# Kernel optimization log

Measured on AMD Instinct MI355X. Metric: run time of the kernel, lower is better.

The kernel has to match this reference:

```python
import jax, jax.numpy as jnp
import numpy as np

N, Z, H, W, R = 8192, 1024, 2048, 64, 8
SCALE = 1.0


def setup_inputs() -> dict:
    key = jax.random.key(0)
    ks = jax.random.split(key, 8)
    return {
        "z": jax.random.normal(ks[0], (N, Z), dtype=jnp.float32),
        "a_idx": jax.random.randint(ks[1], (N,), 0, W),
        "h_pre": jax.random.normal(ks[2], (N, H), dtype=jnp.float32),
        "out_pre": jax.random.normal(ks[3], (N, Z), dtype=jnp.float32),
        "a1": jax.random.normal(ks[4], (W, R, Z), dtype=jnp.float32) * 0.02,
        "b1": jax.random.normal(ks[5], (W, H, R), dtype=jnp.float32) * 0.02,
        "a2": jax.random.normal(ks[6], (W, R, H), dtype=jnp.float32) * 0.02,
        "b2": jax.random.normal(ks[7], (W, Z, R), dtype=jnp.float32) * 0.02,
    }


def reference(z, a_idx, h_pre, out_pre, a1, b1, a2, b2):
    # Gather per-token expert LoRA factors (faithful to torch indexing a1[a_idx])
    A1 = a1[a_idx]                                  # [N, R, Z]
    B1 = b1[a_idx]                                  # [N, H, R]
    t1 = jnp.einsum('nd,nrd->nr', z, A1)            # [N, R]
    d1 = jnp.einsum('nr,nhr->nh', t1, B1) * SCALE   # [N, H]
    h = jax.nn.silu(h_pre + d1)                     # [N, H]
    A2 = a2[a_idx]                                  # [N, R, H]
    B2 = b2[a_idx]                                  # [N, Z, R]
    t2 = jnp.einsum('nh,nrh->nr', h, A2)            # [N, R]
    d2 = jnp.einsum('nr,ndr->nd', t2, B2) * SCALE   # [N, Z]
    return out_pre + d2
```

## Files before the change

### kernel.cpp

```cpp
#include <hip/hip_runtime.h>
#include <stdint.h>


constexpr int Zd = 1024;
constexpr int Hd = 2048;
constexpr int Rr = 8;
constexpr int Wn = 64;
constexpr int TB = 16;
constexpr int TW = 2;
constexpr int NT = 512;
constexpr int HC = 256;
constexpr int NCHUNK = Hd / HC;
constexpr float kScale = 1.0f;


__global__ __launch_bounds__(1024) void bucket_kernel(
    const int* __restrict__ a_idx, int N, int* __restrict__ ws)
{
    __shared__ int hist[Wn];
    __shared__ int cursor[Wn];
    const int t = threadIdx.x;
    if (t < Wn) hist[t] = 0;
    __syncthreads();
    for (int i = t; i < N; i += 1024) atomicAdd(&hist[a_idx[i]], 1);
    __syncthreads();

    if (t < Wn) {
        const int c = hist[t];
        int scan = c;
#pragma unroll
        for (int off = 1; off < 64; off <<= 1) {
            const int v = __shfl_up(scan, off, 64);
            if (t >= off) scan += v;
        }
        const int base = scan - c;

        const int nb_e = (c + TB - 1) / TB;
        int bs = nb_e;
#pragma unroll
        for (int off = 1; off < 64; off <<= 1) {
            const int v = __shfl_up(bs, off, 64);
            if (t >= off) bs += v;
        }
        const int bstart = bs - nb_e;
        if (t == Wn - 1) ws[0] = bs;
        cursor[t] = base;

        int4* btab = (int4*)(ws + 16 + N);
        for (int s = 0, k = 0; s < c; s += TB, ++k)
            btab[bstart + k] = make_int4(t, base + s, min(TB, c - s), 0);
    }
    __syncthreads();
    int* order = ws + 16;
    for (int i = t; i < N; i += 1024) {
        const int pos = atomicAdd(&cursor[a_idx[i]], 1);
        order[pos] = i;
    }
}

__device__ __forceinline__ float wave_allreduce(float v) {
#pragma unroll
    for (int off = 1; off < 64; off <<= 1)
        v += __shfl_xor(v, off, 64);
    return v;
}

__device__ __forceinline__ float dot8(const float* t, float4 w0, float4 w1) {
    return fmaf(t[0], w0.x, fmaf(t[1], w0.y, fmaf(t[2], w0.z, fmaf(t[3], w0.w,
           fmaf(t[4], w1.x, fmaf(t[5], w1.y, fmaf(t[6], w1.z, t[7] * w1.w)))))));
}

__device__ __forceinline__ float silu(float x) {
    return x * __builtin_amdgcn_rcpf(1.f + __expf(-x));
}

__device__ __forceinline__ int swz(int o) {
    return o ^ (((o >> 7) & 7) << 4);
}

__device__ __forceinline__ void stage16(const void* g, void* l) {
    __builtin_amdgcn_global_load_lds(
        (const __attribute__((address_space(1))) uint32_t*)g,
        (__attribute__((address_space(3))) uint32_t*)l, 16, 0, 0);
}

#define WAITVM(N) asm volatile("s_waitcnt vmcnt(" #N ")" ::: "memory")
#define SYNC()    asm volatile("s_waitcnt lgkmcnt(0)\ns_barrier" ::: "memory")

__global__ __launch_bounds__(NT, 4) void lora_main(
    const float* __restrict__ z,
    const float* __restrict__ h_pre,
    const float* __restrict__ out_pre,
    const float* __restrict__ a1,
    const float* __restrict__ b1,
    const float* __restrict__ a2,
    const float* __restrict__ b2,
    float* __restrict__ out,
    const int* __restrict__ ws, int N)
{
    __shared__ float s_a1[Rr * Zd];
    __shared__ float s_b1[3][HC * Rr];
    __shared__ float s_a2[3][Rr * HC];

    const int cpx = gridDim.x >> 3;
    const int lb  = (blockIdx.x & 7) * cpx + (blockIdx.x >> 3);
    if (lb >= ws[0]) return;

    const int4 desc = ((const int4*)(ws + 16 + N))[lb];
    const int e = desc.x, start = desc.y, cnt = desc.z;
    const int* order = ws + 16;

    const int t    = threadIdx.x;
    const int wave = t >> 6;
    const int lane = t & 63;

    bool val[TW];
    int  tok[TW];
#pragma unroll
    for (int k = 0; k < TW; ++k) {
        const int idx = wave * TW + k;
        val[k] = (idx < cnt);
        tok[k] = order[start + (val[k] ? idx : 0)];
    }

    const char*  a1e = (const char*)(a1 + (size_t)e * (Rr * Zd));
    const char*  b1e = (const char*)(b1 + (size_t)e * (Hd * Rr));
    const float* a2e = a2 + (size_t)e * (Rr * Hd);
    const char*  b2e = (const char*)(b2 + (size_t)e * (Zd * Rr));

#pragma unroll
    for (int i = 0; i < 4; ++i) {
        const int o = (i * NT + t) * 16;
        stage16(a1e + o, (char*)s_a1 + (i * NT + wave * 64) * 16);
    }
#pragma unroll
    for (int c0 = 0; c0 < 2; ++c0) {
        const int o = t * 16;
        stage16(b1e + (size_t)(c0 * HC) * Rr * 4 + swz(o),
                (char*)s_b1[c0] + wave * 1024);
        stage16(a2e + wave * Hd + c0 * HC + lane * 4,
                (char*)s_a2[c0] + wave * 1024);
    }
    WAITVM(4);
    SYNC();

    float p[TW][Rr];
#pragma unroll
    for (int k = 0; k < TW; ++k)
#pragma unroll
        for (int r = 0; r < Rr; ++r) p[k][r] = 0.f;

#pragma unroll
    for (int i = 0; i < Zd / 4 / 64; ++i) {
        const int c = lane + i * 64;
        float4 zv[TW];
#pragma unroll
        for (int k = 0; k < TW; ++k)
            zv[k] = *(const float4*)(z + (size_t)tok[k] * Zd + 4 * c);
#pragma unroll
        for (int r = 0; r < Rr; ++r) {
            const float4 w = *(const float4*)(s_a1 + r * Zd + 4 * c);
#pragma unroll
            for (int k = 0; k < TW; ++k)
                p[k][r] = fmaf(zv[k].x, w.x, fmaf(zv[k].y, w.y,
                          fmaf(zv[k].z, w.z, fmaf(zv[k].w, w.w, p[k][r]))));
        }
    }
    float t1[TW][Rr];
#pragma unroll
    for (int k = 0; k < TW; ++k)
#pragma unroll
        for (int r = 0; r < Rr; ++r) t1[k][r] = wave_allreduce(p[k][r]);

    SYNC();

#pragma unroll
    for (int i = 0; i < 4; ++i) {
        const int o = (i * NT + t) * 16;
        stage16(b2e + swz(o), (char*)s_a1 + (i * NT + wave * 64) * 16);
    }

    float q[TW][Rr];
#pragma unroll
    for (int k = 0; k < TW; ++k)
#pragma unroll
        for (int r = 0; r < Rr; ++r) q[k][r] = 0.f;

#pragma unroll
    for (int kc = 0; kc < NCHUNK; ++kc) {
        if (kc < 2)      { WAITVM(6); }
        else if (kc < 7) { WAITVM(2); }
        else             { WAITVM(0); }
        SYNC();

        if (kc + 2 < NCHUNK) {
            const int nb = (kc + 2) % 3;
            const int hb = (kc + 2) * HC;
            const int o = t * 16;
            stage16(b1e + (size_t)hb * Rr * 4 + swz(o),
                    (char*)s_b1[nb] + wave * 1024);
            stage16(a2e + wave * Hd + hb + lane * 4,
                    (char*)s_a2[nb] + wave * 1024);
        }

        const int cur = kc % 3;
        const int cc = kc * 64 + lane;
        float4 hv[TW];
#pragma unroll
        for (int k = 0; k < TW; ++k)
            hv[k] = *(const float4*)(h_pre + (size_t)tok[k] * Hd + 4 * cc);

        float sv[TW][4];
#pragma unroll
        for (int j = 0; j < 4; ++j) {
            const int o0 = lane * 128 + j * 32;
            const float4 w0 = *(const float4*)((const char*)s_b1[cur] + swz(o0));
            const float4 w1 = *(const float4*)((const char*)s_b1[cur] + swz(o0 + 16));
#pragma unroll
            for (int k = 0; k < TW; ++k) {
                const float x = (&hv[k].x)[j] + dot8(t1[k], w0, w1) * kScale;
                sv[k][j] = silu(x);
            }
        }
#pragma unroll
        for (int r = 0; r < Rr; ++r) {
            const float4 aw = *(const float4*)(s_a2[cur] + r * HC + lane * 4);
#pragma unroll
            for (int k = 0; k < TW; ++k)
                q[k][r] = fmaf(sv[k][0], aw.x, fmaf(sv[k][1], aw.y,
                          fmaf(sv[k][2], aw.z, fmaf(sv[k][3], aw.w, q[k][r]))));
        }
    }

    float t2[TW][Rr];
#pragma unroll
    for (int k = 0; k < TW; ++k)
#pragma unroll
        for (int r = 0; r < Rr; ++r) t2[k][r] = wave_allreduce(q[k][r]) * kScale;

#pragma unroll
    for (int i = 0; i < Zd / 4 / 64; ++i) {
        const int c = lane + i * 64;
        float4 ov[TW];
#pragma unroll
        for (int k = 0; k < TW; ++k)
            ov[k] = *(const float4*)(out_pre + (size_t)tok[k] * Zd + 4 * c);
        float4 res[TW];
#pragma unroll
        for (int j = 0; j < 4; ++j) {
            const int o0 = c * 128 + j * 32;
            const float4 w0 = *(const float4*)((const char*)s_a1 + swz(o0));
            const float4 w1 = *(const float4*)((const char*)s_a1 + swz(o0 + 16));
#pragma unroll
            for (int k = 0; k < TW; ++k)
                (&res[k].x)[j] = (&ov[k].x)[j] + dot8(t2[k], w0, w1);
        }
#pragma unroll
        for (int k = 0; k < TW; ++k)
            if (val[k]) *(float4*)(out + (size_t)tok[k] * Zd + 4 * c) = res[k];
    }
}

extern "C" void kernel_launch(void* const* d_in, const int* in_sizes, int n_in,
                              void* d_out, int out_size, void* d_ws, size_t ws_size,
                              hipStream_t stream) {
    const float* z       = (const float*)d_in[0];
    const int*   a_idx   = (const int*)d_in[1];
    const float* h_pre   = (const float*)d_in[2];
    const float* out_pre = (const float*)d_in[3];
    const float* a1      = (const float*)d_in[4];
    const float* b1      = (const float*)d_in[5];
    const float* a2      = (const float*)d_in[6];
    const float* b2      = (const float*)d_in[7];
    float* out = (float*)d_out;

    const int N = in_sizes[1];

    bucket_kernel<<<1, 1024, 0, stream>>>(a_idx, N, (int*)d_ws);

    int nwg = N / TB + Wn;
    nwg = (nwg + 7) & ~7;
    lora_main<<<nwg, NT, 0, stream>>>(z, h_pre, out_pre, a1, b1, a2, b2, out,
                                      (const int*)d_ws, N);
}
```

Before: 57.83 us.

## Read A1/B2 directly from global, prefetch h_pre, vectorize bucket histogram

Removes the 32KB LDS staging of a1 and b2, so both are read straight from global/L2. This shrinks shared memory so more blocks fit per CU, and the occupancy hint rises from 4 to 6. h_pre rows are double-buffered one chunk ahead, and the vmcnt waits are retuned to match the new count of in-flight loads. The bucket kernel now reads a_idx as int4; the trade-off is redundant global reads of the weights by every wave and fewer registers per thread.

```diff
diff --git a/kernel.cpp b/kernel.cpp
--- a/kernel.cpp
+++ b/kernel.cpp
@@ -22,7 +22,12 @@
     const int t = threadIdx.x;
     if (t < Wn) hist[t] = 0;
     __syncthreads();
-    for (int i = t; i < N; i += 1024) atomicAdd(&hist[a_idx[i]], 1);
+    for (int i = t; i < N / 4; i += 1024) {
+        const int4 v = ((const int4*)a_idx)[i];
+        atomicAdd(&hist[v.x], 1); atomicAdd(&hist[v.y], 1);
+        atomicAdd(&hist[v.z], 1); atomicAdd(&hist[v.w], 1);
+    }
+    for (int i = (N & ~3) + t; i < N; i += 1024) atomicAdd(&hist[a_idx[i]], 1);
     __syncthreads();
 
     if (t < Wn) {
@@ -52,10 +57,15 @@
     }
     __syncthreads();
     int* order = ws + 16;
-    for (int i = t; i < N; i += 1024) {
-        const int pos = atomicAdd(&cursor[a_idx[i]], 1);
-        order[pos] = i;
-    }
+    for (int i = t; i < N / 4; i += 1024) {
+        const int4 v = ((const int4*)a_idx)[i];
+        order[atomicAdd(&cursor[v.x], 1)] = 4 * i + 0;
+        order[atomicAdd(&cursor[v.y], 1)] = 4 * i + 1;
+        order[atomicAdd(&cursor[v.z], 1)] = 4 * i + 2;
+        order[atomicAdd(&cursor[v.w], 1)] = 4 * i + 3;
+    }
+    for (int i = (N & ~3) + t; i < N; i += 1024)
+        order[atomicAdd(&cursor[a_idx[i]], 1)] = i;
 }
 
 __device__ __forceinline__ float wave_allreduce(float v) {
@@ -87,7 +97,7 @@
 #define WAITVM(N) asm volatile("s_waitcnt vmcnt(" #N ")" ::: "memory")
 #define SYNC()    asm volatile("s_waitcnt lgkmcnt(0)\ns_barrier" ::: "memory")
 
-__global__ __launch_bounds__(NT, 4) void lora_main(
+__global__ __launch_bounds__(NT, 6) void lora_main(
     const float* __restrict__ z,
     const float* __restrict__ h_pre,
     const float* __restrict__ out_pre,
@@ -98,7 +108,6 @@
     float* __restrict__ out,
     const int* __restrict__ ws, int N)
 {
-    __shared__ float s_a1[Rr * Zd];
     __shared__ float s_b1[3][HC * Rr];
     __shared__ float s_a2[3][Rr * HC];
 
@@ -123,16 +132,11 @@
         tok[k] = order[start + (val[k] ? idx : 0)];
     }
 
-    const char*  a1e = (const char*)(a1 + (size_t)e * (Rr * Zd));
-    const char*  b1e = (const char*)(b1 + (size_t)e * (Hd * Rr));
-    const float* a2e = a2 + (size_t)e * (Rr * Hd);
-    const char*  b2e = (const char*)(b2 + (size_t)e * (Zd * Rr));
-
-#pragma unroll
-    for (int i = 0; i < 4; ++i) {
-        const int o = (i * NT + t) * 16;
-        stage16(a1e + o, (char*)s_a1 + (i * NT + wave * 64) * 16);
-    }
+    const float4* A1  = (const float4*)(a1 + (size_t)e * (Rr * Zd));
+    const char*   b1e = (const char*)(b1 + (size_t)e * (Hd * Rr));
+    const float*  a2e = a2 + (size_t)e * (Rr * Hd);
+    const float4* B2  = (const float4*)(b2 + (size_t)e * (Zd * Rr));
+
 #pragma unroll
     for (int c0 = 0; c0 < 2; ++c0) {
         const int o = t * 16;
@@ -141,8 +145,10 @@
         stage16(a2e + wave * Hd + c0 * HC + lane * 4,
                 (char*)s_a2[c0] + wave * 1024);
     }
-    WAITVM(4);
-    SYNC();
+    float4 hv[2][TW];
+#pragma unroll
+    for (int k = 0; k < TW; ++k)
+        hv[0][k] = *(const float4*)(h_pre + (size_t)tok[k] * Hd + 4 * lane);
 
     float p[TW][Rr];
 #pragma unroll
@@ -159,7 +165,7 @@
             zv[k] = *(const float4*)(z + (size_t)tok[k] * Zd + 4 * c);
 #pragma unroll
         for (int r = 0; r < Rr; ++r) {
-            const float4 w = *(const float4*)(s_a1 + r * Zd + 4 * c);
+            const float4 w = A1[r * (Zd / 4) + c];
 #pragma unroll
             for (int k = 0; k < TW; ++k)
                 p[k][r] = fmaf(zv[k].x, w.x, fmaf(zv[k].y, w.y,
@@ -172,14 +178,6 @@
 #pragma unroll
         for (int r = 0; r < Rr; ++r) t1[k][r] = wave_allreduce(p[k][r]);
 
-    SYNC();
-
-#pragma unroll
-    for (int i = 0; i < 4; ++i) {
-        const int o = (i * NT + t) * 16;
-        stage16(b2e + swz(o), (char*)s_a1 + (i * NT + wave * 64) * 16);
-    }
-
     float q[TW][Rr];
 #pragma unroll
     for (int k = 0; k < TW; ++k)
@@ -188,9 +186,8 @@
 
 #pragma unroll
     for (int kc = 0; kc < NCHUNK; ++kc) {
-        if (kc < 2)      { WAITVM(6); }
-        else if (kc < 7) { WAITVM(2); }
-        else             { WAITVM(0); }
+        if (kc < NCHUNK - 1) { WAITVM(4); }
+        else                 { WAITVM(2); }
         SYNC();
 
         if (kc + 2 < NCHUNK) {
@@ -202,14 +199,15 @@
             stage16(a2e + wave * Hd + hb + lane * 4,
                     (char*)s_a2[nb] + wave * 1024);
         }
+        if (kc + 1 < NCHUNK) {
+            const int cc = (kc + 1) * 64 + lane;
+#pragma unroll
+            for (int k = 0; k < TW; ++k)
+                hv[(kc + 1) & 1][k] =
+                    *(const float4*)(h_pre + (size_t)tok[k] * Hd + 4 * cc);
+        }
 
         const int cur = kc % 3;
-        const int cc = kc * 64 + lane;
-        float4 hv[TW];
-#pragma unroll
-        for (int k = 0; k < TW; ++k)
-            hv[k] = *(const float4*)(h_pre + (size_t)tok[k] * Hd + 4 * cc);
-
         float sv[TW][4];
 #pragma unroll
         for (int j = 0; j < 4; ++j) {
@@ -218,7 +216,7 @@
             const float4 w1 = *(const float4*)((const char*)s_b1[cur] + swz(o0 + 16));
 #pragma unroll
             for (int k = 0; k < TW; ++k) {
-                const float x = (&hv[k].x)[j] + dot8(t1[k], w0, w1) * kScale;
+                const float x = (&hv[kc & 1][k].x)[j] + dot8(t1[k], w0, w1) * kScale;
                 sv[k][j] = silu(x);
             }
         }
@@ -248,9 +246,8 @@
         float4 res[TW];
 #pragma unroll
         for (int j = 0; j < 4; ++j) {
-            const int o0 = c * 128 + j * 32;
-            const float4 w0 = *(const float4*)((const char*)s_a1 + swz(o0));
-            const float4 w1 = *(const float4*)((const char*)s_a1 + swz(o0 + 16));
+            const float4 w0 = B2[(4 * c + j) * 2 + 0];
+            const float4 w1 = B2[(4 * c + j) * 2 + 1];
 #pragma unroll
             for (int k = 0; k < TW; ++k)
                 (&res[k].x)[j] = (&ov[k].x)[j] + dot8(t2[k], w0, w1);
```

Result: slower. 75.38 us (+30.3%).
